# Kernel optimization log

Measured on AMD Instinct MI355X. Metric: run time of the kernel, lower is better.

## Reference

```python
import jax, jax.numpy as jnp
import numpy as np

B = 262144
D = 128          # state_dim
L = 8            # levels
STOP_THRESHOLD = 0.6
LN_EPS = 1e-5


def setup_inputs() -> dict:
    key = jax.random.key(0)
    ks = jax.random.split(key, 4)
    signal = jax.random.normal(ks[0], (B, D), dtype=jnp.float32)
    previous = jax.random.normal(ks[1], (B, D), dtype=jnp.float32)
    # nn.Linear default init: U(-1/sqrt(fan_in), 1/sqrt(fan_in)), fan_in = 2D
    bound = 1.0 / np.sqrt(2 * D)
    Wp = jax.random.uniform(ks[2], (L, 2 * D, D), jnp.float32, -bound, bound)  # projection weight (in, out)
    bp = jax.random.uniform(ks[3], (L, D), jnp.float32, -bound, bound)
    # _reset_parameters: gate weight zeros, gate bias -1.2; stop head all zeros
    Wg = jnp.zeros((L, 2 * D, D), jnp.float32)
    bg = jnp.full((L, D), -1.2, jnp.float32)
    Ws = jnp.zeros((L, 2 * D, 1), jnp.float32)
    bs = jnp.zeros((L, 1), jnp.float32)
    gamma = jnp.ones((L, D), jnp.float32)   # LayerNorm weight
    beta = jnp.zeros((L, D), jnp.float32)   # LayerNorm bias
    return {"signal": signal, "previous": previous, "Wp": Wp, "bp": bp,
            "Wg": Wg, "bg": bg, "Ws": Ws, "bs": bs, "gamma": gamma, "beta": beta}


def _layernorm(x, gamma, beta):
    mu = jnp.mean(x, axis=-1, keepdims=True)
    var = jnp.mean(jnp.square(x - mu), axis=-1, keepdims=True)
    return (x - mu) * jax.lax.rsqrt(var + LN_EPS) * gamma + beta


def reference(signal, previous, Wp, bp, Wg, bg, Ws, bs, gamma, beta):
    levels = jnp.arange(1, L + 1, dtype=signal.dtype)

    def step(carry, xs):
        current, acc, active, depth, smass = carry
        Wp_l, bp_l, Wg_l, bg_l, Ws_l, bs_l, g_l, b_l, lvl = xs
        joined = jnp.concatenate([current, previous], axis=-1)           # [B, 2D]
        gate = jax.nn.sigmoid(joined @ Wg_l + bg_l)                      # [B, D]
        candidate = jnp.tanh(joined @ Wp_l + bp_l)                       # [B, D]
        updated = _layernorm(current + gate * (candidate - current), g_l, b_l)
        joined2 = jnp.concatenate([updated, previous], axis=-1)
        adequacy = jax.nn.sigmoid(joined2 @ Ws_l + bs_l)                 # [B, 1]
        stop_prob = jax.nn.sigmoid((adequacy - STOP_THRESHOLD) * 10.0)
        stop_mass = active * stop_prob
        acc = acc + stop_mass * updated
        active = active * (1.0 - stop_prob)
        depth = depth + stop_mass * lvl
        smass = smass + stop_mass
        stats = (jnp.mean(gate, axis=-1),                                # gate mean  [B]
                 jnp.linalg.norm(updated - current, axis=-1),            # delta norm [B]
                 adequacy[:, 0])                                         # adequacy   [B]
        return (updated, acc, active, depth, smass), stats

    init = (signal,
            jnp.zeros_like(signal),
            jnp.ones((signal.shape[0], 1), signal.dtype),
            jnp.zeros((signal.shape[0], 1), signal.dtype),
            jnp.zeros((signal.shape[0], 1), signal.dtype))
    (current, acc, active, depth, smass), (gates, deltas, adeqs) = jax.lax.scan(
        step, init, (Wp, bp, Wg, bg, Ws, bs, gamma, beta, levels))

    accumulated = acc + active * current
    stop_depth = depth + active * float(L)
    gate_mean = jnp.mean(gates, axis=0)       # mean over levels -> [B]
    delta_mean = jnp.mean(deltas, axis=0)
    adequacy_mean = jnp.mean(adeqs, axis=0)
    return (accumulated, gate_mean, delta_mean,
            stop_depth[:, 0], smass[:, 0], adequacy_mean)
```

## Files before the change

### kernel.cpp

```cpp
#include <hip/hip_runtime.h>
#include <math.h>

#define NB 262144
#define ND 128
#define NL 8

typedef __bf16 bf16x8 __attribute__((ext_vector_type(8)));
typedef float  f32x4  __attribute__((ext_vector_type(4)));

union BFP { unsigned int u; __bf16 h[2]; unsigned short s[2]; };

__device__ __forceinline__ float sigm(float x){ return 1.0f/(1.0f + __expf(-x)); }
__device__ __forceinline__ float tanhfast(float x){
  float t = __expf(-2.0f*fabsf(x));
  return copysignf((1.0f - t)/(1.0f + t), x);
}
__device__ __forceinline__ float red16(float v){
  v += __shfl_xor(v, 1);
  v += __shfl_xor(v, 2);
  v += __shfl_xor(v, 4);
  v += __shfl_xor(v, 8);
  return v;
}
__device__ __forceinline__ unsigned short bfbits(float f){
  BFP x; x.h[0] = (__bf16)f; return x.s[0];
}
__device__ __forceinline__ unsigned int pk2(float a, float b){
  BFP x; x.h[0]=(__bf16)a; x.h[1]=(__bf16)b; return x.u;
}
__device__ __forceinline__ void gload16(const void* g, void* s){
  __builtin_amdgcn_global_load_lds((const __attribute__((address_space(1))) unsigned int*)g,
                                   (__attribute__((address_space(3))) unsigned int*)s,
                                   16, 0, 0);
}

__global__ void repack_w(const float* __restrict__ Wp, const float* __restrict__ Wg,
                         uint4* __restrict__ dst){
  int t = blockIdx.x*256 + threadIdx.x;
  int lane = t & 63;
  int frag = t >> 6;
  int cf = frag & 7, kf = (frag >> 3) & 7, mat = (frag >> 6) & 1, l = frag >> 7;
  const float* W = mat ? Wp : Wg;
  int k = kf*32 + (lane >> 4)*8;
  int n = cf*16 + (lane & 15);
  const float* src = W + (l*256 + k)*ND + n;
  bf16x8 v;
#pragma unroll
  for (int j=0;j<8;++j) v[j] = (__bf16)src[j*ND];
  dst[((l*2 + mat)*64 + kf*8 + cf)*64 + lane] = __builtin_bit_cast(uint4, v);
}

__global__ void prevdot_k(const float* __restrict__ previous, const float* __restrict__ Ws,
                          const float* __restrict__ bs, float* __restrict__ pdot){
  int t = blockIdx.x*256 + threadIdx.x;
  int row = t >> 4, g = t & 15;
  const float* p = previous + (size_t)row*ND + g*8;
  float4 a = *(const float4*)p;
  float4 b = *(const float4*)(p+4);
#pragma unroll
  for (int l=0;l<NL;++l){
    const float* w = Ws + l*256 + 128 + g*8;
    float s = a.x*w[0] + a.y*w[1] + a.z*w[2] + a.w*w[3]
            + b.x*w[4] + b.y*w[5] + b.z*w[6] + b.w*w[7];
    s += __shfl_xor(s,1); s += __shfl_xor(s,2); s += __shfl_xor(s,4); s += __shfl_xor(s,8);
    if (g==0) pdot[row*NL + l] = s + bs[l];
  }
}

__global__ __launch_bounds__(256, 2)
void fused_k(const float* __restrict__ signal, const float* __restrict__ previous,
             const float* __restrict__ bp, const float* __restrict__ bg,
             const float* __restrict__ Ws, const float* __restrict__ gamma,
             const float* __restrict__ beta,
             const uint4* __restrict__ wpk, const float* __restrict__ pdot,
             float* __restrict__ out)
{
  __shared__ unsigned short tile[64*128];
  __shared__ uint4 wbuf[4096];

  const int tid  = threadIdx.x;
  const int w    = tid >> 6;
  const int lane = tid & 63;
  const int llo  = lane & 15;
  const int lhi  = lane >> 4;
  const int rbase = w * 16;
  const int row0  = blockIdx.x * 64;

  bf16x8 prevA[4];
  {
    int row = row0 + rbase + llo;
#pragma unroll
    for (int kf=0; kf<4; ++kf){
      const float* p = previous + (size_t)row*ND + kf*32 + lhi*8;
      float4 f0 = *(const float4*)p;
      float4 f1 = *(const float4*)(p+4);
      bf16x8 v;
      v[0]=(__bf16)f0.x; v[1]=(__bf16)f0.y; v[2]=(__bf16)f0.z; v[3]=(__bf16)f0.w;
      v[4]=(__bf16)f1.x; v[5]=(__bf16)f1.y; v[6]=(__bf16)f1.z; v[7]=(__bf16)f1.w;
      prevA[kf] = v;
    }
  }

  float curC[8][4];
  f32x4 accv[8];
  float active[4], depth[4], smass[4], gsum[4], dsum[4], asum[4];
#pragma unroll
  for (int cf=0; cf<8; ++cf){
    accv[cf] = (f32x4){0.f,0.f,0.f,0.f};
#pragma unroll
    for (int r=0; r<4; ++r){
      int row = row0 + rbase + lhi*4 + r;
      curC[cf][r] = signal[(size_t)row*ND + cf*16 + llo];
    }
  }
#pragma unroll
  for (int r=0; r<4; ++r){
    active[r]=1.f; depth[r]=0.f; smass[r]=0.f;
    gsum[r]=0.f; dsum[r]=0.f; asum[r]=0.f;
  }

#pragma unroll 1
  for (int l=0; l<NL; ++l){
    {
      const char* src = (const char*)wpk + (size_t)(l*2 + 0)*65536;
      char* dstb = (char*)wbuf;
#pragma unroll
      for (int i=0;i<16;++i){
        int off = i*4096 + tid*16;
        gload16(src + off, dstb + off);
      }
    }
#pragma unroll
    for (int cf=0; cf<8; ++cf)
#pragma unroll
      for (int r=0; r<4; ++r){
        int rowl = rbase + lhi*4 + r;
        int byte = ((cf*16 + llo)*2) ^ ((rowl & 7) << 4);
        tile[rowl*128 + (byte>>1)] = bfbits(curC[cf][r]);
      }
    asm volatile("s_waitcnt lgkmcnt(0)" ::: "memory");
    __builtin_amdgcn_sched_barrier(0);
    bf16x8 curA[4];
    {
      int rowl = rbase + llo;
      const char* base = (const char*)tile + rowl*256;
      int sw = (rowl & 7) << 4;
#pragma unroll
      for (int kf=0; kf<4; ++kf){
        int byte = (kf*64 + lhi*16) ^ sw;
        curA[kf] = __builtin_bit_cast(bf16x8, *(const uint4*)(base + byte));
      }
    }
    __syncthreads();

    f32x4 pacc[8];
    auto zero_acc = [&](){
#pragma unroll
      for (int cf=0; cf<8; ++cf) pacc[cf] = (f32x4){0.f,0.f,0.f,0.f};
    };
    auto run_gemm = [&](){
#pragma unroll
      for (int kf=0; kf<4; ++kf){
        bf16x8 a = curA[kf];
#pragma unroll
        for (int cf=0; cf<8; ++cf){
          bf16x8 b = __builtin_bit_cast(bf16x8, wbuf[(kf*8+cf)*64 + lane]);
          pacc[cf] = __builtin_amdgcn_mfma_f32_16x16x32_bf16(a, b, pacc[cf], 0,0,0);
        }
      }
#pragma unroll
      for (int kp=0; kp<4; ++kp){
        bf16x8 a = prevA[kp];
#pragma unroll
        for (int cf=0; cf<8; ++cf){
          bf16x8 b = __builtin_bit_cast(bf16x8, wbuf[((kp+4)*8+cf)*64 + lane]);
          pacc[cf] = __builtin_amdgcn_mfma_f32_16x16x32_bf16(a, b, pacc[cf], 0,0,0);
        }
      }
    };

    zero_acc();
    run_gemm();
    __syncthreads();

    {
      const char* src = (const char*)wpk + (size_t)(l*2 + 1)*65536;
      char* dstb = (char*)wbuf;
#pragma unroll
      for (int i=0;i<16;++i){
        int off = i*4096 + tid*16;
        gload16(src + off, dstb + off);
      }
    }

    unsigned int gstash[8][2];
    {
      float gpart[4] = {0.f,0.f,0.f,0.f};
#pragma unroll
      for (int cf=0; cf<8; ++cf){
        float bgv = bg[l*ND + cf*16 + llo];
        float g0 = sigm(pacc[cf][0] + bgv);
        float g1 = sigm(pacc[cf][1] + bgv);
        float g2 = sigm(pacc[cf][2] + bgv);
        float g3 = sigm(pacc[cf][3] + bgv);
        gpart[0]+=g0; gpart[1]+=g1; gpart[2]+=g2; gpart[3]+=g3;
        gstash[cf][0] = pk2(g0,g1);
        gstash[cf][1] = pk2(g2,g3);
      }
#pragma unroll
      for (int r=0; r<4; ++r)
        gsum[r] += red16(gpart[r]) * (1.0f/ND);
    }
    __syncthreads();

    zero_acc();
    run_gemm();
    __syncthreads();

    float s1[4] = {0.f,0.f,0.f,0.f};
    float s2[4] = {0.f,0.f,0.f,0.f};
#pragma unroll
    for (int cf=0; cf<8; ++cf){
      float bpv = bp[l*ND + cf*16 + llo];
#pragma unroll
      for (int r=0; r<4; ++r){
        float cand = tanhfast(pacc[cf][r] + bpv);
        float c = curC[cf][r];
        BFP gp; gp.u = gstash[cf][r>>1];
        float g = (float)gp.h[r&1];
        float x = c + g*(cand - c);
        pacc[cf][r] = x;
        s1[r] += x; s2[r] += x*x;
      }
    }
    float mu[4], inv[4];
#pragma unroll
    for (int r=0; r<4; ++r){
      float m = red16(s1[r]) * (1.0f/ND);
      float q = red16(s2[r]) * (1.0f/ND);
      mu[r] = m;
      inv[r] = rsqrtf(q - m*m + 1e-5f);
    }
    float dpart[4] = {0.f,0.f,0.f,0.f};
    float apart[4] = {0.f,0.f,0.f,0.f};
#pragma unroll
    for (int cf=0; cf<8; ++cf){
      float gm = gamma[l*ND + cf*16 + llo];
      float bt = beta [l*ND + cf*16 + llo];
      float wv = Ws[l*256 + cf*16 + llo];
#pragma unroll
      for (int r=0; r<4; ++r){
        float un = (pacc[cf][r] - mu[r])*inv[r]*gm + bt;
        float c = curC[cf][r];
        float df = un - c;
        dpart[r] += df*df;
        apart[r] += un*wv;
        pacc[cf][r] = un;
      }
    }
    float smrow[4];
#pragma unroll
    for (int r=0; r<4; ++r){
      float dd = red16(dpart[r]);
      float av = red16(apart[r]);
      int row = row0 + rbase + lhi*4 + r;
      float adq = sigm(av + pdot[row*NL + l]);
      float sp  = sigm((adq - 0.6f)*10.0f);
      float sm  = active[r]*sp;
      asum[r] += adq;
      dsum[r] += sqrtf(dd);
      depth[r] += sm * (float)(l+1);
      smass[r] += sm;
      active[r] *= (1.0f - sp);
      smrow[r] = sm;
    }
#pragma unroll
    for (int cf=0; cf<8; ++cf)
#pragma unroll
      for (int r=0; r<4; ++r){
        float un = pacc[cf][r];
        accv[cf][r] += smrow[r]*un;
        curC[cf][r] = un;
      }
  }

#pragma unroll
  for (int cf=0; cf<8; ++cf)
#pragma unroll
    for (int r=0; r<4; ++r){
      int row = row0 + rbase + lhi*4 + r;
      out[(size_t)row*ND + cf*16 + llo] = accv[cf][r] + active[r]*curC[cf][r];
    }
  if (llo == 0){
    const size_t BD = (size_t)NB*ND;
#pragma unroll
    for (int r=0; r<4; ++r){
      int row = row0 + rbase + lhi*4 + r;
      out[BD + row]                = gsum[r]*(1.0f/NL);
      out[BD + NB + row]           = dsum[r]*(1.0f/NL);
      out[BD + 2*(size_t)NB + row] = depth[r] + active[r]*(float)NL;
      out[BD + 3*(size_t)NB + row] = smass[r];
      out[BD + 4*(size_t)NB + row] = asum[r]*(1.0f/NL);
    }
  }
}

extern "C" void kernel_launch(void* const* d_in, const int* in_sizes, int n_in,
                              void* d_out, int out_size, void* d_ws, size_t ws_size,
                              hipStream_t stream){
  const float* signal   = (const float*)d_in[0];
  const float* previous = (const float*)d_in[1];
  const float* Wp    = (const float*)d_in[2];
  const float* bp    = (const float*)d_in[3];
  const float* Wg    = (const float*)d_in[4];
  const float* bg    = (const float*)d_in[5];
  const float* Ws    = (const float*)d_in[6];
  const float* bs    = (const float*)d_in[7];
  const float* gamma = (const float*)d_in[8];
  const float* beta  = (const float*)d_in[9];

  uint4* wpk  = (uint4*)d_ws;
  float* pdot = (float*)((char*)d_ws + (size_t)NL*2*65536);

  repack_w<<<256, 256, 0, stream>>>(Wp, Wg, wpk);
  prevdot_k<<<NB/16, 256, 0, stream>>>(previous, Ws, bs, pdot);
  fused_k<<<NB/64, 256, 0, stream>>>(signal, previous, bp, bg, Ws, gamma, beta,
                                     wpk, pdot, (float*)d_out);
}
```

Measured before the change: 944.7 us.

## Read MFMA weight fragments directly from global memory and use DPP reductions

Drops the shared-memory staging buffer for the packed gate and projection weights. Each wave now loads its B fragments straight from global memory, which should hit in cache, and the block-wide barriers around the staging are removed. This saves LDS space and synchronisation, but every wave now fetches the full 64KB per GEMM, so L2 traffic rises about fourfold and the MFMAs are exposed to global-load latency. The 16-lane row reduction also switches from shfl_xor to DPP quad_perm and row_ror adds.

```diff
diff --git a/kernel.cpp b/kernel.cpp
--- a/kernel.cpp
+++ b/kernel.cpp
@@ -15,11 +15,16 @@
   float t = __expf(-2.0f*fabsf(x));
   return copysignf((1.0f - t)/(1.0f + t), x);
 }
+template<int CTRL>
+__device__ __forceinline__ float dppadd(float v){
+  int y = __builtin_amdgcn_update_dpp(0, __builtin_bit_cast(int, v), CTRL, 0xf, 0xf, true);
+  return v + __builtin_bit_cast(float, y);
+}
 __device__ __forceinline__ float red16(float v){
-  v += __shfl_xor(v, 1);
-  v += __shfl_xor(v, 2);
-  v += __shfl_xor(v, 4);
-  v += __shfl_xor(v, 8);
+  v = dppadd<0xB1>(v);
+  v = dppadd<0x4E>(v);
+  v = dppadd<0x124>(v);
+  v = dppadd<0x128>(v);
   return v;
 }
 __device__ __forceinline__ unsigned short bfbits(float f){
@@ -27,11 +32,6 @@
 }
 __device__ __forceinline__ unsigned int pk2(float a, float b){
   BFP x; x.h[0]=(__bf16)a; x.h[1]=(__bf16)b; return x.u;
-}
-__device__ __forceinline__ void gload16(const void* g, void* s){
-  __builtin_amdgcn_global_load_lds((const __attribute__((address_space(1))) unsigned int*)g,
-                                   (__attribute__((address_space(3))) unsigned int*)s,
-                                   16, 0, 0);
 }
 
 __global__ void repack_w(const float* __restrict__ Wp, const float* __restrict__ Wg,
@@ -76,7 +76,6 @@
              float* __restrict__ out)
 {
   __shared__ unsigned short tile[64*128];
-  __shared__ uint4 wbuf[4096];
 
   const int tid  = threadIdx.x;
   const int w    = tid >> 6;
@@ -121,15 +120,6 @@
 
 #pragma unroll 1
   for (int l=0; l<NL; ++l){
-    {
-      const char* src = (const char*)wpk + (size_t)(l*2 + 0)*65536;
-      char* dstb = (char*)wbuf;
-#pragma unroll
-      for (int i=0;i<16;++i){
-        int off = i*4096 + tid*16;
-        gload16(src + off, dstb + off);
-      }
-    }
 #pragma unroll
     for (int cf=0; cf<8; ++cf)
 #pragma unroll
@@ -151,20 +141,20 @@
         curA[kf] = __builtin_bit_cast(bf16x8, *(const uint4*)(base + byte));
       }
     }
-    __syncthreads();
 
     f32x4 pacc[8];
     auto zero_acc = [&](){
 #pragma unroll
       for (int cf=0; cf<8; ++cf) pacc[cf] = (f32x4){0.f,0.f,0.f,0.f};
     };
-    auto run_gemm = [&](){
+    auto run_gemm = [&](int mat){
+      const uint4* gB = wpk + (size_t)(l*2 + mat)*4096 + lane;
 #pragma unroll
       for (int kf=0; kf<4; ++kf){
         bf16x8 a = curA[kf];
 #pragma unroll
         for (int cf=0; cf<8; ++cf){
-          bf16x8 b = __builtin_bit_cast(bf16x8, wbuf[(kf*8+cf)*64 + lane]);
+          bf16x8 b = __builtin_bit_cast(bf16x8, gB[(kf*8+cf)*64]);
           pacc[cf] = __builtin_amdgcn_mfma_f32_16x16x32_bf16(a, b, pacc[cf], 0,0,0);
         }
       }
@@ -173,25 +163,14 @@
         bf16x8 a = prevA[kp];
 #pragma unroll
         for (int cf=0; cf<8; ++cf){
-          bf16x8 b = __builtin_bit_cast(bf16x8, wbuf[((kp+4)*8+cf)*64 + lane]);
+          bf16x8 b = __builtin_bit_cast(bf16x8, gB[((kp+4)*8+cf)*64]);
           pacc[cf] = __builtin_amdgcn_mfma_f32_16x16x32_bf16(a, b, pacc[cf], 0,0,0);
         }
       }
     };
 
     zero_acc();
-    run_gemm();
-    __syncthreads();
-
-    {
-      const char* src = (const char*)wpk + (size_t)(l*2 + 1)*65536;
-      char* dstb = (char*)wbuf;
-#pragma unroll
-      for (int i=0;i<16;++i){
-        int off = i*4096 + tid*16;
-        gload16(src + off, dstb + off);
-      }
-    }
+    run_gemm(0);
 
     unsigned int gstash[8][2];
     {
@@ -211,11 +190,9 @@
       for (int r=0; r<4; ++r)
         gsum[r] += red16(gpart[r]) * (1.0f/ND);
     }
-    __syncthreads();
 
     zero_acc();
-    run_gemm();
-    __syncthreads();
+    run_gemm(1);
 
     float s1[4] = {0.f,0.f,0.f,0.f};
     float s2[4] = {0.f,0.f,0.f,0.f};
```

After: 2.235 ms. 2.37x slower.
